# Kernel optimization log

Measured on AMD Instinct MI355X. Metric: run time of the kernel, lower is better.

The kernel has to match this reference:

```python
import jax, jax.numpy as jnp
import numpy as np

IN_F, OUT_F = 4096, 11008
B, S = 4, 2048

def setup_inputs() -> dict:
    key = jax.random.key(0)
    k1, k2, k3, k4, k5 = jax.random.split(key, 5)
    x = jax.random.normal(k1, (B, S, IN_F), dtype=jnp.float32)
    packed_weights = jax.random.randint(k2, (OUT_F, IN_F // 2), 0, 256, dtype=jnp.int32)
    scales = jax.random.normal(k3, (OUT_F,), dtype=jnp.float32)
    zero_points = jax.random.randint(k4, (OUT_F,), 0, 15, dtype=jnp.int32)
    bias = jax.random.normal(k5, (1, OUT_F), dtype=jnp.float32)
    return {"x": x, "packed_weights": packed_weights, "scales": scales,
            "zero_points": zero_points, "bias": bias}

def _dequantize(packed_weights, scales, zero_points, dtype):
    # unpack: low nibble first, then high nibble (matches torch stack([low, high], dim=2).view)
    low = packed_weights & 15
    high = (packed_weights >> 4) & 15
    unpacked = jnp.stack([low, high], axis=2).reshape(packed_weights.shape[0], -1)  # [out, in]
    return (unpacked.astype(dtype) - zero_points[:, None].astype(dtype)) * scales[:, None].astype(dtype)

def reference(x, packed_weights, scales, zero_points, bias):
    W = _dequantize(packed_weights, scales, zero_points, x.dtype)  # [out, in]
    out = jnp.einsum('bsi,oi->bso', x, W)  # F.linear
    return out + bias
```

## Files before the change

kernel.cpp:

```cpp
#include <hip/hip_runtime.h>
#include <hip/hip_bf16.h>
#include <stdint.h>

#define IN_F   4096
#define OUT_F  11008
#define M_DIM  8192

#define BM 256
#define BN 256
#define BK 64
#define TM (M_DIM / BM)
#define TN (OUT_F / BN)
#define NWG (TM * TN)
#define KT (IN_F / BK)
#define KC (IN_F / 16)
#define HTB (128 * 64)

typedef __attribute__((ext_vector_type(4))) int   int32x4;
typedef __attribute__((ext_vector_type(8))) short short8;
typedef __attribute__((ext_vector_type(4))) float f32x4;

union Pack8 { __bf16 h[8]; uint4 u; };
union PackI { char c[16]; ::int4 v; };

__device__ inline uint4 pack8_f(float4 f0, float4 f1) {
    Pack8 o;
    o.h[0] = (__bf16)f0.x; o.h[1] = (__bf16)f0.y;
    o.h[2] = (__bf16)f0.z; o.h[3] = (__bf16)f0.w;
    o.h[4] = (__bf16)f1.x; o.h[5] = (__bf16)f1.y;
    o.h[6] = (__bf16)f1.z; o.h[7] = (__bf16)f1.w;
    return o.u;
}

__device__ inline uint4 dequant8(int4 v, float s, float zb) {
    Pack8 o;
    int pv[4] = {v.x, v.y, v.z, v.w};
#pragma unroll
    for (int j = 0; j < 4; ++j) {
        o.h[2 * j]     = (__bf16)fmaf((float)(pv[j] & 15), s, zb);
        o.h[2 * j + 1] = (__bf16)fmaf((float)((pv[j] >> 4) & 15), s, zb);
    }
    return o.u;
}

#define GLOAD_LDS16(g, l)                                                     \
    __builtin_amdgcn_global_load_lds(                                         \
        (const __attribute__((address_space(1))) void*)(g),                   \
        (__attribute__((address_space(3))) void*)(l), 16, 0, 0)

#define BAR()   __builtin_amdgcn_s_barrier()
#define SBAR0() __builtin_amdgcn_sched_barrier(0)
#define VMW(n)  asm volatile("s_waitcnt vmcnt(" #n ")" ::: "memory")

__global__ __launch_bounds__(256) void quant_x_kernel(const float* __restrict__ x,
        char* __restrict__ xq, float* __restrict__ srow) {
    const int row = blockIdx.x;
    const int t   = threadIdx.x;
    const float4* xr = (const float4*)(x + (size_t)row * IN_F) + t * 4;
    float4 v[4];
    float am = 0.f;
#pragma unroll
    for (int j = 0; j < 4; ++j) {
        v[j] = xr[j];
        am = fmaxf(am, fmaxf(fmaxf(fabsf(v[j].x), fabsf(v[j].y)),
                             fmaxf(fabsf(v[j].z), fabsf(v[j].w))));
    }
#pragma unroll
    for (int off = 32; off; off >>= 1) am = fmaxf(am, __shfl_xor(am, off, 64));
    __shared__ float wm4[4];
    if ((t & 63) == 0) wm4[t >> 6] = am;
    __syncthreads();
    am = fmaxf(fmaxf(wm4[0], wm4[1]), fmaxf(wm4[2], wm4[3]));
    const float qs = am > 0.f ? 127.f / am : 0.f;
    if (t == 0) srow[row] = am > 0.f ? am * (1.f / 127.f) : 0.f;
    PackI o;
#pragma unroll
    for (int j = 0; j < 4; ++j) {
        const float* f = (const float*)&v[j];
#pragma unroll
        for (int e = 0; e < 4; ++e) {
            float q = rintf(f[e] * qs);
            q = fminf(127.f, fmaxf(-127.f, q));
            o.c[j * 4 + e] = (char)(int)q;
        }
    }
    ((::int4*)(xq + (size_t)row * IN_F))[t] = o.v;
}

__global__ void deqw_i8_kernel(const int* __restrict__ pw, const int* __restrict__ zps,
                               char* __restrict__ wq, int nChunks) {
    int stride = gridDim.x * blockDim.x;
    for (int c = blockIdx.x * blockDim.x + threadIdx.x; c < nChunks; c += stride) {
        int row = c >> 8;
        int cc  = c & 255;
        int zp  = zps[row];
        const ::int4* p = (const ::int4*)(pw + (size_t)row * (IN_F / 2) + cc * 8);
        ::int4 v0 = p[0], v1 = p[1];
        int pv[8] = {v0.x, v0.y, v0.z, v0.w, v1.x, v1.y, v1.z, v1.w};
        PackI o;
#pragma unroll
        for (int j = 0; j < 8; ++j) {
            o.c[2 * j]     = (char)((pv[j] & 15) - zp);
            o.c[2 * j + 1] = (char)(((pv[j] >> 4) & 15) - zp);
        }
        ((::int4*)wq)[c] = o.v;
    }
}

__device__ inline void stA(char* smem, const uint4* gA, int t, int h, int buf, int wo) {
    GLOAD_LDS16(gA + (size_t)h * 64 * KC + (t & (KT - 1)) * 4,
                smem + ((buf * 2 + 0) * 2 + h) * HTB + wo);
}
__device__ inline void stB(char* smem, const uint4* gB, int t, int h, int buf, int wo) {
    GLOAD_LDS16(gB + (size_t)h * 32 * KC + (t & (KT - 1)) * 4,
                smem + ((buf * 2 + 1) * 2 + h) * HTB + wo);
}

template <int QM>
__device__ inline void read_A(const char* smem, int buf, int wm, int lane, int32x4 (&a)[4]) {
    const char* base = smem + ((buf * 2 + 0) * 2 + QM) * HTB;
    const int pp = lane & 15, q = (lane >> 4) * 16;
#pragma unroll
    for (int mi = 0; mi < 4; ++mi) {
        int row = wm * 64 + mi * 16 + pp;
        a[mi] = *(const int32x4*)(base + row * 64 + (q ^ (((row >> 1) & 3) << 4)));
    }
}

template <int QN>
__device__ inline void read_B(const char* smem, int buf, int wn, int lane, int32x4 (&bq)[2]) {
    const char* base = smem + ((buf * 2 + 1) * 2 + QN) * HTB;
    const int pp = lane & 15, q = (lane >> 4) * 16;
#pragma unroll
    for (int nj = 0; nj < 2; ++nj) {
        int row = wn * 32 + nj * 16 + pp;
        bq[nj] = *(const int32x4*)(base + row * 64 + (q ^ (((row >> 1) & 3) << 4)));
    }
}

template <int QM, int QN>
__device__ inline void mfma8(int32x4 (&a)[4], int32x4 (&bq)[2], int32x4 (&acc)[2][4][2][2]) {
    __builtin_amdgcn_s_setprio(1);
#pragma unroll
    for (int mi = 0; mi < 4; ++mi)
#pragma unroll
        for (int nj = 0; nj < 2; ++nj)
            acc[QM][mi][QN][nj] = __builtin_amdgcn_mfma_i32_16x16x64_i8(
                a[mi], bq[nj], acc[QM][mi][QN][nj], 0, 0, 0);
    __builtin_amdgcn_s_setprio(0);
}

__global__ __launch_bounds__(512, 2) void w4a16_gemm_i8(
    const uint4* __restrict__ xq4, const uint4* __restrict__ wq4,
    const float* __restrict__ srow, const float* __restrict__ scales,
    const float* __restrict__ bias, float* __restrict__ out) {

    extern __shared__ __align__(16) char smem[];

    const int tid  = threadIdx.x;
    const int lane = tid & 63;
    const int wid  = tid >> 6;
    const int wm   = wid >> 2;
    const int wn   = wid & 3;

    const int bid = blockIdx.x;
    const int xcd = bid & 7;
    const int p   = bid >> 3;
    int tm, tn;
    if (p < 160) { int c = p >> 4, q = p & 15; tm = xcd * 4 + (q & 3); tn = c * 4 + (q >> 2); }
    else         { int q = p - 160;            tm = xcd * 4 + (q & 3); tn = 40 + (q >> 2); }
    const int bm0 = tm * BM;
    const int bn0 = tn * BN;

    const int l2  = lane >> 2;
    const int csw = (lane & 3) ^ ((lane >> 3) & 3);
    const uint4* gA = xq4 + (size_t)(bm0 + (wid >> 2) * 128 + (wid & 3) * 16 + l2) * KC + csw;
    const uint4* gB = wq4 + (size_t)(bn0 + (wid >> 1) * 64 + (wid & 1) * 16 + l2) * KC + csw;
    const int wo = wid * 1024;

    int32x4 acc[2][4][2][2];
#pragma unroll
    for (int qm = 0; qm < 2; ++qm)
#pragma unroll
        for (int mi = 0; mi < 4; ++mi)
#pragma unroll
            for (int qn = 0; qn < 2; ++qn)
#pragma unroll
                for (int nj = 0; nj < 2; ++nj) acc[qm][mi][qn][nj] = {0, 0, 0, 0};

    int32x4 a[4];
    int32x4 b[2][2];

    stA(smem, gA, 0, 0, 0, wo); stB(smem, gB, 0, 0, 0, wo);
    stA(smem, gA, 0, 1, 0, wo); stB(smem, gB, 0, 1, 0, wo);
    stA(smem, gA, 1, 0, 1, wo); stB(smem, gB, 1, 0, 1, wo);
    stB(smem, gB, 1, 1, 1, wo); stA(smem, gA, 1, 1, 1, wo);
    VMW(4); SBAR0(); BAR();

    for (int i = 0; i < KT / 2; ++i) {
        const int t2 = 2 * i + 2, t3 = 2 * i + 3;
        read_A<0>(smem, 0, wm, lane, a);
        read_B<0>(smem, 0, wn, lane, b[0]);
        BAR(); mfma8<0, 0>(a, b[0], acc); BAR();
        stA(smem, gA, t2, 0, 0, wo);
        read_B<1>(smem, 0, wn, lane, b[1]);
        BAR(); mfma8<0, 1>(a, b[1], acc); BAR();
        stB(smem, gB, t2, 1, 0, wo);
        read_A<1>(smem, 0, wm, lane, a);
        BAR(); mfma8<1, 0>(a, b[0], acc); BAR();
        stB(smem, gB, t2, 0, 0, wo);
        stA(smem, gA, t2, 1, 0, wo);
        VMW(4); SBAR0(); BAR();
        mfma8<1, 1>(a, b[1], acc); BAR();
        read_A<0>(smem, 1, wm, lane, a);
        read_B<0>(smem, 1, wn, lane, b[0]);
        BAR(); mfma8<0, 0>(a, b[0], acc); BAR();
        stA(smem, gA, t3, 0, 1, wo);
        read_B<1>(smem, 1, wn, lane, b[1]);
        BAR(); mfma8<0, 1>(a, b[1], acc); BAR();
        stB(smem, gB, t3, 1, 1, wo);
        read_A<1>(smem, 1, wm, lane, a);
        BAR(); mfma8<1, 0>(a, b[0], acc); BAR();
        stB(smem, gB, t3, 0, 1, wo);
        stA(smem, gA, t3, 1, 1, wo);
        VMW(4); SBAR0(); BAR();
        mfma8<1, 1>(a, b[1], acc); BAR();
    }
    VMW(0);

#pragma unroll
    for (int qm = 0; qm < 2; ++qm)
#pragma unroll
        for (int mi = 0; mi < 4; ++mi) {
            int row0 = bm0 + wm * 128 + qm * 64 + mi * 16 + (lane >> 4) * 4;
            float sr[4];
#pragma unroll
            for (int rr = 0; rr < 4; ++rr) sr[rr] = srow[row0 + rr];
#pragma unroll
            for (int qn = 0; qn < 2; ++qn)
#pragma unroll
                for (int nj = 0; nj < 2; ++nj) {
                    int col  = bn0 + wn * 64 + qn * 32 + nj * 16 + (lane & 15);
                    float sc = scales[col];
                    float bv = bias[col];
#pragma unroll
                    for (int rr = 0; rr < 4; ++rr)
                        __builtin_nontemporal_store(
                            (float)acc[qm][mi][qn][nj][rr] * (sr[rr] * sc) + bv,
                            &out[(size_t)(row0 + rr) * OUT_F + col]);
                }
        }
}

#define FBM 128
#define FBN 128
#define FTM (M_DIM / FBM)
#define FTN (OUT_F / FBN)
#define FNWG (FTM * FTN)

__global__ __launch_bounds__(256) void w4a16_gemm_fb(
    const float* __restrict__ xf,
    const int* __restrict__ pw,
    const float* __restrict__ scales, const int* __restrict__ zps,
    const float* __restrict__ bias, float* __restrict__ out) {

    __shared__ __align__(16) __bf16 As[FBM * 64];
    __shared__ __align__(16) __bf16 Bs[FBN * 64];

    const int tid  = threadIdx.x;
    const int lane = tid & 63;
    const int wid  = tid >> 6;
    const int wm   = wid >> 1;
    const int wn   = wid & 1;

    int orig = blockIdx.x;
    int wg   = (orig & 7) * (FNWG / 8) + (orig >> 3);
    const int bm0 = (wg / FTN) * FBM;
    const int bn0 = (wg % FTN) * FBN;

    f32x4 acc[4][4];
#pragma unroll
    for (int i = 0; i < 4; ++i)
#pragma unroll
        for (int j = 0; j < 4; ++j) acc[i][j] = {0.f, 0.f, 0.f, 0.f};

    for (int kt = 0; kt < IN_F / 64; ++kt) {
#pragma unroll
        for (int i = 0; i < 4; ++i) {
            int ci  = i * 256 + tid;
            int row = ci >> 3, c8 = ci & 7;
            const float4* pp = (const float4*)(xf + (size_t)(bm0 + row) * IN_F + kt * 64 + c8 * 8);
            uint4 d = pack8_f(pp[0], pp[1]);
            *(uint4*)((char*)As + row * 128 + ((c8 * 16) ^ ((row & 7) << 4))) = d;
        }
#pragma unroll
        for (int i = 0; i < 4; ++i) {
            int ci  = i * 256 + tid;
            int row = ci >> 3, c8 = ci & 7;
            int r    = bn0 + row;
            float s  = scales[r];
            float zb = -s * (float)zps[r];
            int4 v = *(const int4*)(pw + (size_t)r * (IN_F / 2) + kt * 32 + c8 * 4);
            uint4 d = dequant8(v, s, zb);
            *(uint4*)((char*)Bs + row * 128 + ((c8 * 16) ^ ((row & 7) << 4))) = d;
        }
        __syncthreads();

#pragma unroll
        for (int kk = 0; kk < 2; ++kk) {
            short8 a[4], b[4];
#pragma unroll
            for (int mi = 0; mi < 4; ++mi) {
                int row = wm * 64 + mi * 16 + (lane & 15);
                a[mi] = *(const short8*)((const char*)As + row * 128 +
                                         ((kk * 64 + (lane >> 4) * 16) ^ ((row & 7) << 4)));
            }
#pragma unroll
            for (int ni = 0; ni < 4; ++ni) {
                int row = wn * 64 + ni * 16 + (lane & 15);
                b[ni] = *(const short8*)((const char*)Bs + row * 128 +
                                         ((kk * 64 + (lane >> 4) * 16) ^ ((row & 7) << 4)));
            }
#pragma unroll
            for (int mi = 0; mi < 4; ++mi)
#pragma unroll
                for (int ni = 0; ni < 4; ++ni)
                    acc[mi][ni] = __builtin_amdgcn_mfma_f32_16x16x32_bf16(a[mi], b[ni], acc[mi][ni], 0, 0, 0);
        }
        __syncthreads();
    }

#pragma unroll
    for (int ni = 0; ni < 4; ++ni) {
        int col  = bn0 + wn * 64 + ni * 16 + (lane & 15);
        float bv = bias[col];
#pragma unroll
        for (int mi = 0; mi < 4; ++mi) {
            int row0 = bm0 + wm * 64 + mi * 16 + (lane >> 4) * 4;
#pragma unroll
            for (int r = 0; r < 4; ++r)
                out[(size_t)(row0 + r) * OUT_F + col] = acc[mi][ni][r] + bv;
        }
    }
}

extern "C" void kernel_launch(void* const* d_in, const int* in_sizes, int n_in,
                              void* d_out, int out_size, void* d_ws, size_t ws_size,
                              hipStream_t stream) {
    const float* x      = (const float*)d_in[0];
    const int* pw       = (const int*)d_in[1];
    const float* scales = (const float*)d_in[2];
    const int* zps      = (const int*)d_in[3];
    const float* bias   = (const float*)d_in[4];
    float* out          = (float*)d_out;

    const size_t xq_bytes = (size_t)M_DIM * IN_F;
    const size_t sr_bytes = 65536;
    const size_t wq_bytes = (size_t)OUT_F * IN_F;
    const bool predeq = ws_size >= xq_bytes + sr_bytes + wq_bytes;

    if (predeq) {
        char*  xq   = (char*)d_ws;
        float* srow = (float*)((char*)d_ws + xq_bytes);
        char*  wq   = (char*)d_ws + xq_bytes + sr_bytes;
        quant_x_kernel<<<dim3(M_DIM), dim3(256), 0, stream>>>(x, xq, srow);
        deqw_i8_kernel<<<dim3(2048), dim3(256), 0, stream>>>(pw, zps, wq, OUT_F * (IN_F / 16));
        (void)hipFuncSetAttribute((const void*)w4a16_gemm_i8,
                                  hipFuncAttributeMaxDynamicSharedMemorySize, 65536);
        w4a16_gemm_i8<<<dim3(NWG), dim3(512), 65536, stream>>>(
            (const uint4*)xq, (const uint4*)wq, srow, scales, bias, out);
    } else {
        w4a16_gemm_fb<<<dim3(FNWG), dim3(256), 0, stream>>>(x, pw, scales, zps, bias, out);
    }
}
```

Measured before the change: 434.4 us.

## Merge MFMA groups per A half and reschedule global-to-LDS loads

Each A fragment now drives a single 16-instruction MFMA burst against both B halves, in place of two 8-instruction bursts, which halves the barriers per K-tile. The global-to-LDS load schedule is reordered: the second A half of the next tile is issued inside the loop rather than in the prologue, and the vmcnt wait drops to 3. The aim is to cut barrier and sync overhead and overlap memory with compute better. The cost is that both B fragments stay live at once, which raises register pressure, and the new load order must still respect the buffer hazards.

```diff
diff --git a/kernel.cpp b/kernel.cpp
--- a/kernel.cpp
+++ b/kernel.cpp
@@ -138,15 +138,21 @@
     }
 }
 
-template <int QM, int QN>
-__device__ inline void mfma8(int32x4 (&a)[4], int32x4 (&bq)[2], int32x4 (&acc)[2][4][2][2]) {
+template <int QM>
+__device__ inline void mfma16both(int32x4 (&a)[4], int32x4 (&b0)[2], int32x4 (&b1)[2],
+                                  int32x4 (&acc)[2][4][2][2]) {
     __builtin_amdgcn_s_setprio(1);
 #pragma unroll
-    for (int mi = 0; mi < 4; ++mi)
+    for (int mi = 0; mi < 4; ++mi) {
 #pragma unroll
         for (int nj = 0; nj < 2; ++nj)
-            acc[QM][mi][QN][nj] = __builtin_amdgcn_mfma_i32_16x16x64_i8(
-                a[mi], bq[nj], acc[QM][mi][QN][nj], 0, 0, 0);
+            acc[QM][mi][0][nj] = __builtin_amdgcn_mfma_i32_16x16x64_i8(
+                a[mi], b0[nj], acc[QM][mi][0][nj], 0, 0, 0);
+#pragma unroll
+        for (int nj = 0; nj < 2; ++nj)
+            acc[QM][mi][1][nj] = __builtin_amdgcn_mfma_i32_16x16x64_i8(
+                a[mi], b1[nj], acc[QM][mi][1][nj], 0, 0, 0);
+    }
     __builtin_amdgcn_s_setprio(0);
 }
 
@@ -192,39 +198,35 @@
     int32x4 b[2][2];
 
     stA(smem, gA, 0, 0, 0, wo); stB(smem, gB, 0, 0, 0, wo);
-    stA(smem, gA, 0, 1, 0, wo); stB(smem, gB, 0, 1, 0, wo);
+    stB(smem, gB, 0, 1, 0, wo); stA(smem, gA, 0, 1, 0, wo);
     stA(smem, gA, 1, 0, 1, wo); stB(smem, gB, 1, 0, 1, wo);
-    stB(smem, gB, 1, 1, 1, wo); stA(smem, gA, 1, 1, 1, wo);
-    VMW(4); SBAR0(); BAR();
+    stB(smem, gB, 1, 1, 1, wo);
+    VMW(3); SBAR0(); BAR();
 
     for (int i = 0; i < KT / 2; ++i) {
-        const int t2 = 2 * i + 2, t3 = 2 * i + 3;
+        const int to = 2 * i + 1, t2 = 2 * i + 2, t3 = 2 * i + 3;
         read_A<0>(smem, 0, wm, lane, a);
         read_B<0>(smem, 0, wn, lane, b[0]);
-        BAR(); mfma8<0, 0>(a, b[0], acc); BAR();
+        read_B<1>(smem, 0, wn, lane, b[1]);
+        stA(smem, gA, to, 1, 1, wo);
+        BAR(); mfma16both<0>(a, b[0], b[1], acc); BAR();
+        read_A<1>(smem, 0, wm, lane, a);
         stA(smem, gA, t2, 0, 0, wo);
-        read_B<1>(smem, 0, wn, lane, b[1]);
-        BAR(); mfma8<0, 1>(a, b[1], acc); BAR();
+        stB(smem, gB, t2, 0, 0, wo);
         stB(smem, gB, t2, 1, 0, wo);
-        read_A<1>(smem, 0, wm, lane, a);
-        BAR(); mfma8<1, 0>(a, b[0], acc); BAR();
-        stB(smem, gB, t2, 0, 0, wo);
-        stA(smem, gA, t2, 1, 0, wo);
-        VMW(4); SBAR0(); BAR();
-        mfma8<1, 1>(a, b[1], acc); BAR();
+        VMW(3); SBAR0(); BAR();
+        mfma16both<1>(a, b[0], b[1], acc); BAR();
         read_A<0>(smem, 1, wm, lane, a);
         read_B<0>(smem, 1, wn, lane, b[0]);
-        BAR(); mfma8<0, 0>(a, b[0], acc); BAR();
+        read_B<1>(smem, 1, wn, lane, b[1]);
+        stA(smem, gA, t2, 1, 0, wo);
+        BAR(); mfma16both<0>(a, b[0], b[1], acc); BAR();
+        read_A<1>(smem, 1, wm, lane, a);
         stA(smem, gA, t3, 0, 1, wo);
-        read_B<1>(smem, 1, wn, lane, b[1]);
-        BAR(); mfma8<0, 1>(a, b[1], acc); BAR();
+        stB(smem, gB, t3, 0, 1, wo);
         stB(smem, gB, t3, 1, 1, wo);
-        read_A<1>(smem, 1, wm, lane, a);
-        BAR(); mfma8<1, 0>(a, b[0], acc); BAR();
-        stB(smem, gB, t3, 0, 1, wo);
-        stA(smem, gA, t3, 1, 1, wo);
-        VMW(4); SBAR0(); BAR();
-        mfma8<1, 1>(a, b[1], acc); BAR();
+        VMW(3); SBAR0(); BAR();
+        mfma16both<1>(a, b[0], b[1], acc); BAR();
     }
     VMW(0);
 
```

Result: no change. 441.3 us (+1.6%).

## Shrink GEMM N-tile to 128 with triple-buffered single-barrier K loop

Applied to the files above, without the earlier changes.

Changes the int8 MFMA GEMM from a 256x256 tile with a double-buffered, heavily barriered 8-phase schedule to a 256x128 tile with a 3-stage LDS ring buffer. Each K step issues one prefetch two tiles ahead, waits once, then each wave does a 4x4 MFMA block. The aim is fewer barriers and deeper prefetch, at the cost of less operand reuse per tile, more global and L2 traffic, and twice as many workgroups. The XCD-aware tile mapping is rescaled to match.

```diff
diff --git a/kernel.cpp b/kernel.cpp
--- a/kernel.cpp
+++ b/kernel.cpp
@@ -7,14 +7,14 @@
 #define M_DIM  8192
 
 #define BM 256
-#define BN 256
-#define BK 64
+#define BN 128
 #define TM (M_DIM / BM)
 #define TN (OUT_F / BN)
 #define NWG (TM * TN)
-#define KT (IN_F / BK)
+#define KT (IN_F / 64)
 #define KC (IN_F / 16)
-#define HTB (128 * 64)
+#define TILE_B 24576
+#define B_OFF  16384
 
 typedef __attribute__((ext_vector_type(4))) int   int32x4;
 typedef __attribute__((ext_vector_type(8))) short short8;
@@ -107,49 +107,6 @@
     }
 }
 
-__device__ inline void stA(char* smem, const uint4* gA, int t, int h, int buf, int wo) {
-    GLOAD_LDS16(gA + (size_t)h * 64 * KC + (t & (KT - 1)) * 4,
-                smem + ((buf * 2 + 0) * 2 + h) * HTB + wo);
-}
-__device__ inline void stB(char* smem, const uint4* gB, int t, int h, int buf, int wo) {
-    GLOAD_LDS16(gB + (size_t)h * 32 * KC + (t & (KT - 1)) * 4,
-                smem + ((buf * 2 + 1) * 2 + h) * HTB + wo);
-}
-
-template <int QM>
-__device__ inline void read_A(const char* smem, int buf, int wm, int lane, int32x4 (&a)[4]) {
-    const char* base = smem + ((buf * 2 + 0) * 2 + QM) * HTB;
-    const int pp = lane & 15, q = (lane >> 4) * 16;
-#pragma unroll
-    for (int mi = 0; mi < 4; ++mi) {
-        int row = wm * 64 + mi * 16 + pp;
-        a[mi] = *(const int32x4*)(base + row * 64 + (q ^ (((row >> 1) & 3) << 4)));
-    }
-}
-
-template <int QN>
-__device__ inline void read_B(const char* smem, int buf, int wn, int lane, int32x4 (&bq)[2]) {
-    const char* base = smem + ((buf * 2 + 1) * 2 + QN) * HTB;
-    const int pp = lane & 15, q = (lane >> 4) * 16;
-#pragma unroll
-    for (int nj = 0; nj < 2; ++nj) {
-        int row = wn * 32 + nj * 16 + pp;
-        bq[nj] = *(const int32x4*)(base + row * 64 + (q ^ (((row >> 1) & 3) << 4)));
-    }
-}
-
-template <int QM, int QN>
-__device__ inline void mfma8(int32x4 (&a)[4], int32x4 (&bq)[2], int32x4 (&acc)[2][4][2][2]) {
-    __builtin_amdgcn_s_setprio(1);
-#pragma unroll
-    for (int mi = 0; mi < 4; ++mi)
-#pragma unroll
-        for (int nj = 0; nj < 2; ++nj)
-            acc[QM][mi][QN][nj] = __builtin_amdgcn_mfma_i32_16x16x64_i8(
-                a[mi], bq[nj], acc[QM][mi][QN][nj], 0, 0, 0);
-    __builtin_amdgcn_s_setprio(0);
-}
-
 __global__ __launch_bounds__(512, 2) void w4a16_gemm_i8(
     const uint4* __restrict__ xq4, const uint4* __restrict__ wq4,
     const float* __restrict__ srow, const float* __restrict__ scales,
@@ -160,96 +117,96 @@
     const int tid  = threadIdx.x;
     const int lane = tid & 63;
     const int wid  = tid >> 6;
-    const int wm   = wid >> 2;
-    const int wn   = wid & 3;
+    const int wm   = wid >> 1;
+    const int wn   = wid & 1;
 
     const int bid = blockIdx.x;
     const int xcd = bid & 7;
     const int p   = bid >> 3;
     int tm, tn;
-    if (p < 160) { int c = p >> 4, q = p & 15; tm = xcd * 4 + (q & 3); tn = c * 4 + (q >> 2); }
-    else         { int q = p - 160;            tm = xcd * 4 + (q & 3); tn = 40 + (q >> 2); }
+    if (p < 336) { int c = p >> 4, q = p & 15; tm = xcd * 4 + (q & 3); tn = c * 4 + (q >> 2); }
+    else         { int q = p - 336;            tm = xcd * 4 + (q & 3); tn = 84 + (q >> 2); }
     const int bm0 = tm * BM;
     const int bn0 = tn * BN;
 
-    const int l2  = lane >> 2;
+    const int r4  = (wid << 4) + (lane >> 2);
     const int csw = (lane & 3) ^ ((lane >> 3) & 3);
-    const uint4* gA = xq4 + (size_t)(bm0 + (wid >> 2) * 128 + (wid & 3) * 16 + l2) * KC + csw;
-    const uint4* gB = wq4 + (size_t)(bn0 + (wid >> 1) * 64 + (wid & 1) * 16 + l2) * KC + csw;
-    const int wo = wid * 1024;
-
-    int32x4 acc[2][4][2][2];
-#pragma unroll
-    for (int qm = 0; qm < 2; ++qm)
+    const uint4* gA  = xq4 + (size_t)(bm0 + r4) * KC + csw;
+    const uint4* gA2 = gA + (size_t)128 * KC;
+    const uint4* gB  = wq4 + (size_t)(bn0 + r4) * KC + csw;
+    const int wo = wid << 10;
+
+    int32x4 acc[4][4];
+#pragma unroll
+    for (int mi = 0; mi < 4; ++mi)
+#pragma unroll
+        for (int nj = 0; nj < 4; ++nj) acc[mi][nj] = {0, 0, 0, 0};
+
+#pragma unroll
+    for (int t = 0; t < 2; ++t) {
+        int off = t * TILE_B + wo;
+        GLOAD_LDS16(gA + t * 4, smem + off);
+        GLOAD_LDS16(gA2 + t * 4, smem + off + 8192);
+        GLOAD_LDS16(gB + t * 4, smem + t * TILE_B + B_OFF + wo);
+    }
+
+    int bR = 0, bS = 2;
+    for (int kt = 0; kt < KT; ++kt) {
+        const int tc = ((kt + 2) & (KT - 1)) * 4;
+        {
+            int off = bS * TILE_B + wo;
+            GLOAD_LDS16(gA + tc, smem + off);
+            GLOAD_LDS16(gA2 + tc, smem + off + 8192);
+            GLOAD_LDS16(gB + tc, smem + bS * TILE_B + B_OFF + wo);
+        }
+        VMW(6); SBAR0(); BAR(); SBAR0();
+
+        const char* base = smem + bR * TILE_B;
+        int32x4 a[4], b[4];
+#pragma unroll
+        for (int mi = 0; mi < 4; ++mi) {
+            int row = wm * 64 + mi * 16 + (lane & 15);
+            a[mi] = *(const int32x4*)(base + row * 64 +
+                     (((lane >> 4) * 16) ^ (((row >> 1) & 3) << 4)));
+        }
+#pragma unroll
+        for (int nj = 0; nj < 4; ++nj) {
+            int row = wn * 64 + nj * 16 + (lane & 15);
+            b[nj] = *(const int32x4*)(base + B_OFF + row * 64 +
+                     (((lane >> 4) * 16) ^ (((row >> 1) & 3) << 4)));
+        }
+        __builtin_amdgcn_s_setprio(1);
 #pragma unroll
         for (int mi = 0; mi < 4; ++mi)
 #pragma unroll
-            for (int qn = 0; qn < 2; ++qn)
-#pragma unroll
-                for (int nj = 0; nj < 2; ++nj) acc[qm][mi][qn][nj] = {0, 0, 0, 0};
-
-    int32x4 a[4];
-    int32x4 b[2][2];
-
-    stA(smem, gA, 0, 0, 0, wo); stB(smem, gB, 0, 0, 0, wo);
-    stA(smem, gA, 0, 1, 0, wo); stB(smem, gB, 0, 1, 0, wo);
-    stA(smem, gA, 1, 0, 1, wo); stB(smem, gB, 1, 0, 1, wo);
-    stB(smem, gB, 1, 1, 1, wo); stA(smem, gA, 1, 1, 1, wo);
-    VMW(4); SBAR0(); BAR();
-
-    for (int i = 0; i < KT / 2; ++i) {
-        const int t2 = 2 * i + 2, t3 = 2 * i + 3;
-        read_A<0>(smem, 0, wm, lane, a);
-        read_B<0>(smem, 0, wn, lane, b[0]);
-        BAR(); mfma8<0, 0>(a, b[0], acc); BAR();
-        stA(smem, gA, t2, 0, 0, wo);
-        read_B<1>(smem, 0, wn, lane, b[1]);
-        BAR(); mfma8<0, 1>(a, b[1], acc); BAR();
-        stB(smem, gB, t2, 1, 0, wo);
-        read_A<1>(smem, 0, wm, lane, a);
-        BAR(); mfma8<1, 0>(a, b[0], acc); BAR();
-        stB(smem, gB, t2, 0, 0, wo);
-        stA(smem, gA, t2, 1, 0, wo);
-        VMW(4); SBAR0(); BAR();
-        mfma8<1, 1>(a, b[1], acc); BAR();
-        read_A<0>(smem, 1, wm, lane, a);
-        read_B<0>(smem, 1, wn, lane, b[0]);
-        BAR(); mfma8<0, 0>(a, b[0], acc); BAR();
-        stA(smem, gA, t3, 0, 1, wo);
-        read_B<1>(smem, 1, wn, lane, b[1]);
-        BAR(); mfma8<0, 1>(a, b[1], acc); BAR();
-        stB(smem, gB, t3, 1, 1, wo);
-        read_A<1>(smem, 1, wm, lane, a);
-        BAR(); mfma8<1, 0>(a, b[0], acc); BAR();
-        stB(smem, gB, t3, 0, 1, wo);
-        stA(smem, gA, t3, 1, 1, wo);
-        VMW(4); SBAR0(); BAR();
-        mfma8<1, 1>(a, b[1], acc); BAR();
+            for (int nj = 0; nj < 4; ++nj)
+                acc[mi][nj] = __builtin_amdgcn_mfma_i32_16x16x64_i8(
+                    a[mi], b[nj], acc[mi][nj], 0, 0, 0);
+        __builtin_amdgcn_s_setprio(0);
+        BAR();
+
+        int t = bR; bR = (bR == 2) ? 0 : bR + 1; bS = (bS == 2) ? 0 : bS + 1; (void)t;
     }
     VMW(0);
 
 #pragma unroll
-    for (int qm = 0; qm < 2; ++qm)
-#pragma unroll
-        for (int mi = 0; mi < 4; ++mi) {
-            int row0 = bm0 + wm * 128 + qm * 64 + mi * 16 + (lane >> 4) * 4;
-            float sr[4];
-#pragma unroll
-            for (int rr = 0; rr < 4; ++rr) sr[rr] = srow[row0 + rr];
-#pragma unroll
-            for (int qn = 0; qn < 2; ++qn)
-#pragma unroll
-                for (int nj = 0; nj < 2; ++nj) {
-                    int col  = bn0 + wn * 64 + qn * 32 + nj * 16 + (lane & 15);
-                    float sc = scales[col];
-                    float bv = bias[col];
-#pragma unroll
-                    for (int rr = 0; rr < 4; ++rr)
-                        __builtin_nontemporal_store(
-                            (float)acc[qm][mi][qn][nj][rr] * (sr[rr] * sc) + bv,
-                            &out[(size_t)(row0 + rr) * OUT_F + col]);
-                }
-        }
+    for (int mi = 0; mi < 4; ++mi) {
+        int row0 = bm0 + wm * 64 + mi * 16 + (lane >> 4) * 4;
+        float sr[4];
+#pragma unroll
+        for (int rr = 0; rr < 4; ++rr) sr[rr] = srow[row0 + rr];
+#pragma unroll
+        for (int nj = 0; nj < 4; ++nj) {
+            int col  = bn0 + wn * 64 + nj * 16 + (lane & 15);
+            float sc = scales[col];
+            float bv = bias[col];
+#pragma unroll
+            for (int rr = 0; rr < 4; ++rr)
+                __builtin_nontemporal_store(
+                    (float)acc[mi][nj][rr] * (sr[rr] * sc) + bv,
+                    &out[(size_t)(row0 + rr) * OUT_F + col]);
+        }
+    }
 }
 
 #define FBM 128
@@ -366,8 +323,8 @@
         quant_x_kernel<<<dim3(M_DIM), dim3(256), 0, stream>>>(x, xq, srow);
         deqw_i8_kernel<<<dim3(2048), dim3(256), 0, stream>>>(pw, zps, wq, OUT_F * (IN_F / 16));
         (void)hipFuncSetAttribute((const void*)w4a16_gemm_i8,
-                                  hipFuncAttributeMaxDynamicSharedMemorySize, 65536);
-        w4a16_gemm_i8<<<dim3(NWG), dim3(512), 65536, stream>>>(
+                                  hipFuncAttributeMaxDynamicSharedMemorySize, 3 * TILE_B);
+        w4a16_gemm_i8<<<dim3(NWG), dim3(512), 3 * TILE_B, stream>>>(
             (const uint4*)xq, (const uint4*)wq, srow, scales, bias, out);
     } else {
         w4a16_gemm_fb<<<dim3(FNWG), dim3(256), 0, stream>>>(x, pw, scales, zps, bias, out);
```

Result: no change. 442.0 us (+1.8%).
